# Performance work log

Hardware: AMD Instinct MI355X
Metric: run time of the kernel (lower is better)

## Reference

```python
import jax, jax.numpy as jnp
import numpy as np

B, N, D, H, A = 1024, 16, 64, 64, 64
TAU = 0.01   # gumbel-softmax temperature from the source
EPS = 1e-10


def setup_inputs() -> dict:
    key = jax.random.key(0)
    ks = jax.random.split(key, 23)

    def rn(k, shape, s=0.05):
        return jax.random.normal(k, shape, dtype=jnp.float32) * s

    return {
        "obs": jax.random.normal(ks[0], (B, N, D), dtype=jnp.float32),
        "hidden_state": jax.random.normal(ks[1], (B * N, A), dtype=jnp.float32),
        "gumbel_u": jax.random.uniform(ks[2], (B * N * (N - 1), 2), dtype=jnp.float32,
                                       minval=1e-6, maxval=1.0 - 1e-6),
        "W_enc": rn(ks[3], (D, H)), "b_enc": rn(ks[4], (H,)),
        "Wih_f": rn(ks[5], (3 * H, 2 * H)), "Whh_f": rn(ks[6], (3 * H, H)),
        "bih_f": rn(ks[7], (3 * H,)), "bhh_f": rn(ks[8], (3 * H,)),
        "Wih_b": rn(ks[9], (3 * H, 2 * H)), "Whh_b": rn(ks[10], (3 * H, H)),
        "bih_b": rn(ks[11], (3 * H,)), "bhh_b": rn(ks[12], (3 * H,)),
        "W_hard": rn(ks[13], (2 * H, 2)), "b_hard": rn(ks[14], (2,)),
        "Wq": rn(ks[15], (H, A)), "Wk": rn(ks[16], (H, A)),
        "Wv": rn(ks[17], (H, A)), "b_v": rn(ks[18], (A,)),
        "Wih_c": rn(ks[19], (3 * A, A)), "Whh_c": rn(ks[20], (3 * A, A)),
        "bih_c": rn(ks[21], (3 * A,)), "bhh_c": rn(ks[22], (3 * A,)),
    }


def _gru_scan(x_seq, Wih, Whh, bih, bhh):
    # x_seq: [T, BN, 2H]; PyTorch GRU gate order r, z, n. Input projection
    # for all timesteps is precomputed (one big GEMM) outside the scan.
    gi = jnp.einsum('tbd,gd->tbg', x_seq, Wih) + bih  # [T, BN, 3H]
    h0 = jnp.zeros((x_seq.shape[1], Whh.shape[1]), x_seq.dtype)

    def step(h, gi_t):
        gh = h @ Whh.T + bhh
        i_r, i_z, i_n = jnp.split(gi_t, 3, axis=-1)
        h_r, h_z, h_n = jnp.split(gh, 3, axis=-1)
        r = jax.nn.sigmoid(i_r + h_r)
        z = jax.nn.sigmoid(i_z + h_z)
        n = jnp.tanh(i_n + r * h_n)
        h_new = (1.0 - z) * n + z * h
        return h_new, h_new

    _, out = jax.lax.scan(step, h0, gi)
    return out  # [T, BN, H]


def _gru_cell(x, h, Wih, Whh, bih, bhh):
    gi = x @ Wih.T + bih
    gh = h @ Whh.T + bhh
    i_r, i_z, i_n = jnp.split(gi, 3, axis=-1)
    h_r, h_z, h_n = jnp.split(gh, 3, axis=-1)
    r = jax.nn.sigmoid(i_r + h_r)
    z = jax.nn.sigmoid(i_z + h_z)
    n = jnp.tanh(i_n + r * h_n)
    return (1.0 - z) * n + z * h


def reference(obs, hidden_state, gumbel_u, W_enc, b_enc,
              Wih_f, Whh_f, bih_f, bhh_f, Wih_b, Whh_b, bih_b, bhh_b,
              W_hard, b_hard, Wq, Wk, Wv, b_v,
              Wih_c, Whh_c, bih_c, bhh_c):
    b, n, d = obs.shape
    h_enc = jax.nn.relu(obs @ W_enc + b_enc)          # [B, N, H]
    h_flat = h_enc.reshape(-1, H)                      # [B*N, H]

    # static neighbor index table: row i lists all j != i
    j_idx = np.array([[j for j in range(n) if j != i] for i in range(n)])  # [N, N-1]

    # pairwise concat features, vectorized (replaces the double python loop)
    h_j = h_enc[:, j_idx]                               # [B, N, N-1, H]
    h_i = jnp.broadcast_to(h_enc[:, :, None, :], h_j.shape)
    pair = jnp.concatenate([h_i, h_j], axis=-1)        # [B, N, N-1, 2H]
    input_hard = pair.transpose(2, 0, 1, 3).reshape(n - 1, b * n, 2 * H)

    # bidirectional GRU over the N-1 neighbor axis
    out_f = _gru_scan(input_hard, Wih_f, Whh_f, bih_f, bhh_f)
    out_b = _gru_scan(input_hard[::-1], Wih_b, Whh_b, bih_b, bhh_b)[::-1]
    h_hard = jnp.concatenate([out_f, out_b], axis=-1)  # [N-1, B*N, 2H]
    h_hard = h_hard.transpose(1, 0, 2).reshape(-1, 2 * H)

    # hard gate: gumbel-softmax (soft sample, tau=0.01), take channel 1
    logits = h_hard @ W_hard + b_hard                   # [B*N*(N-1), 2]
    g = -jnp.log(-jnp.log(gumbel_u + EPS) + EPS)
    hard = jax.nn.softmax((logits + g) / TAU, axis=-1)
    hard_w = hard[:, 1].reshape(b, n, n - 1)            # [B, N, N-1]

    # scaled dot-product attention over neighbors j != i
    q = (h_flat @ Wq).reshape(b, n, A)
    k = (h_flat @ Wk).reshape(b, n, A)
    v = jax.nn.relu(h_flat @ Wv + b_v).reshape(b, n, A)
    k_j = k[:, j_idx]                                   # [B, N, N-1, A]
    v_j = v[:, j_idx]
    score = jnp.einsum('bna,bnja->bnj', q, k_j) / float(np.sqrt(A))
    soft = jax.nn.softmax(score, axis=-1)
    x = jnp.einsum('bnja,bnj->bna', v_j, soft * hard_w).reshape(b * n, A)

    return _gru_cell(x, hidden_state, Wih_c, Whh_c, bih_c, bhh_c)
```

## Files before the change

kernel.cpp:

```cpp
#include <hip/hip_runtime.h>
#include <hip/hip_bf16.h>
#include <stdint.h>

#define NNODE 16384
#define TAU_ 0.01f
#define EPSG 1e-10f

#define OFF_WENC 0
#define OFF_BENC 4096
#define OFF_WIHF_H 4160
#define OFF_WIHF_L 16448
#define OFF_WHHF_H 28736
#define OFF_BIHF 41024
#define OFF_BHHF 41216
#define OFF_WIHB_H 41408
#define OFF_WIHB_L 53696
#define OFF_WHHB_H 65984
#define OFF_BIHB 78272
#define OFF_BHHB 78464
#define OFF_WHARD 78656
#define OFF_BHARD 78912
#define OFF_WQT_H 78914
#define OFF_WQT_L 80962
#define OFF_WKT_H 83010
#define OFF_WKT_L 85058
#define OFF_WVT_H 87106
#define OFF_WVT_L 89154
#define OFF_BV 91202
#define OFF_WIHC_H 91266
#define OFF_WIHC_L 97410
#define OFF_WHHC_H 103554
#define OFF_WHHC_L 109698
#define OFF_BIHC 115842
#define OFF_BHHC 116034
#define OFF_WENCT_H 118784
#define OFF_WENCT_L 120832
#define OFF_YF 131072
#define OFF_YB (OFF_YF + 491520)
#define WS_FLOATS (OFF_YB + 491520)

typedef float  v4f __attribute__((ext_vector_type(4)));
typedef short  v8s __attribute__((ext_vector_type(8)));

__device__ __forceinline__ float rcpf(float x){ return __builtin_amdgcn_rcpf(x); }
__device__ __forceinline__ float sigf(float x){ return rcpf(1.0f + __expf(-x)); }
__device__ __forceinline__ float tanhfast(float x){ return 1.0f - 2.0f*rcpf(__expf(2.0f*x)+1.0f); }
__device__ __forceinline__ unsigned short f2bf(float f){
  __hip_bfloat16 h = __float2bfloat16(f);
  return *reinterpret_cast<unsigned short*>(&h);
}
__device__ __forceinline__ float bf2f(unsigned short u){
  union { unsigned int i; float f; } v; v.i = ((unsigned int)u) << 16; return v.f;
}

struct Prep {
  const float* s[20];
  int n[20];
  int o[20];
};
__global__ void k_prep(Prep p, float* __restrict__ ws){
  int a = blockIdx.y;
  int i = blockIdx.x * blockDim.x + threadIdx.x;
  if (i < p.n[a]) ws[p.o[a] + i] = p.s[a][i];
}

__global__ void k_prep2(const float* __restrict__ wenc,
                        const float* __restrict__ wihf, const float* __restrict__ wihb,
                        const float* __restrict__ whhf, const float* __restrict__ whhb,
                        const float* __restrict__ wq,   const float* __restrict__ wk,
                        const float* __restrict__ wv,   const float* __restrict__ wihc,
                        const float* __restrict__ whhc,
                        float* __restrict__ ws){
  int a = blockIdx.y;
  int i = blockIdx.x * blockDim.x + threadIdx.x;
  if (a == 0 || (a >= 5 && a <= 7)){
    if (i < 4096){
      const float* src = (a==0) ? wenc : (a==5) ? wq : (a==6) ? wk : wv;
      int oh = (a==0) ? OFF_WENCT_H : (a==5) ? OFF_WQT_H : (a==6) ? OFF_WKT_H : OFF_WVT_H;
      int ol = (a==0) ? OFF_WENCT_L : oh + 2048;
      float x = src[((i & 63) << 6) | (i >> 6)];
      unsigned short h = f2bf(x);
      unsigned short l = f2bf(x - bf2f(h));
      ((unsigned short*)(ws + oh))[i] = h;
      ((unsigned short*)(ws + ol))[i] = l;
    }
  } else if (a == 1 || a == 2){
    if (i < 24576){
      float x = (a == 1 ? wihf : wihb)[i];
      unsigned short h = f2bf(x);
      unsigned short l = f2bf(x - bf2f(h));
      ((unsigned short*)(ws + (a == 1 ? OFF_WIHF_H : OFF_WIHB_H)))[i] = h;
      ((unsigned short*)(ws + (a == 1 ? OFF_WIHF_L : OFF_WIHB_L)))[i] = l;
    }
  } else if (a == 3 || a == 4){
    if (i < 12288){
      float x = (a == 3 ? whhf : whhb)[i];
      ((unsigned short*)(ws + (a == 3 ? OFF_WHHF_H : OFF_WHHB_H)))[i] = f2bf(x);
    }
  } else {
    if (i < 12288){
      float x = (a == 8 ? wihc : whhc)[i];
      unsigned short h = f2bf(x);
      unsigned short l = f2bf(x - bf2f(h));
      int oh = (a == 8 ? OFF_WIHC_H : OFF_WHHC_H);
      ((unsigned short*)(ws + oh))[i] = h;
      ((unsigned short*)(ws + oh + 6144))[i] = l;
    }
  }
}

__global__ __launch_bounds__(256, 2) void k_main(const float* __restrict__ obs,
                                                 const float* __restrict__ hid,
                                                 const float* __restrict__ gum,
                                                 float* __restrict__ ws,
                                                 float* __restrict__ out){
  __shared__ float smem[10176];
  float* s_u2 = smem;
  unsigned short* s_B = (unsigned short*)(smem + 6272);
  unsigned short* s_obs_h = s_B;
  unsigned short* s_obs_l = s_B + 1152;
  float* s_red = smem + 9088;
  float* s_y   = smem + 9216;
  float* s_q  = smem;
  float* s_k  = smem + 1088;
  float* s_v  = smem + 2176;
  float* s_co = smem + 3264;

  const int tid = threadIdx.x;
  const int nl  = tid & 63;
  const int grp = __builtin_amdgcn_readfirstlane(tid >> 6);
  const int dir = grp >> 1;
  const int lw  = grp & 1;
  const int hi2 = grp;
  const int q4  = nl >> 4;
  const int i_c = nl & 15;
  const int node = i_c;
  const int base = blockIdx.x * 16;

  {
    float4 a = *(const float4*)&obs[base*64 + tid*4];
    int nn = tid >> 4, d0 = (tid & 15)*4;
    unsigned short hh[4], ll[4];
    float xs[4] = {a.x,a.y,a.z,a.w};
    #pragma unroll
    for (int e = 0; e < 4; e++){
      hh[e] = f2bf(xs[e]);
      ll[e] = f2bf(xs[e] - bf2f(hh[e]));
    }
    *(uint2*)&s_obs_h[nn*72 + d0] = make_uint2((unsigned)hh[0] | ((unsigned)hh[1]<<16),
                                               (unsigned)hh[2] | ((unsigned)hh[3]<<16));
    *(uint2*)&s_obs_l[nn*72 + d0] = make_uint2((unsigned)ll[0] | ((unsigned)ll[1]<<16),
                                               (unsigned)ll[2] | ((unsigned)ll[3]<<16));
  }
  __syncthreads();

  const float* benc = ws + OFF_BENC;
  const unsigned short* wtH = (const unsigned short*)(ws + OFF_WENCT_H);
  const unsigned short* wtL = (const unsigned short*)(ws + OFF_WENCT_L);
  v4f dEnc;
  {
    v8s obH[2], obL[2];
    #pragma unroll
    for (int kc = 0; kc < 2; kc++){
      int ba = node*72 + kc*32 + q4*8;
      obH[kc] = *(const v8s*)&s_obs_h[ba];
      obL[kc] = *(const v8s*)&s_obs_l[ba];
    }
    float4 bi = *(const float4*)&benc[16*hi2 + 4*q4];
    v4f d = (v4f){bi.x, bi.y, bi.z, bi.w};
    #pragma unroll
    for (int kc = 0; kc < 2; kc++){
      int aa = (16*hi2 + i_c)*64 + kc*32 + q4*8;
      v8s aH = *(const v8s*)&wtH[aa];
      v8s aL = *(const v8s*)&wtL[aa];
      d = __builtin_amdgcn_mfma_f32_16x16x32_bf16(aH, obH[kc], d, 0,0,0);
      d = __builtin_amdgcn_mfma_f32_16x16x32_bf16(aH, obL[kc], d, 0,0,0);
      d = __builtin_amdgcn_mfma_f32_16x16x32_bf16(aL, obH[kc], d, 0,0,0);
    }
    dEnc = d;
  }
  __syncthreads();
  {
    unsigned short hh[4], ll[4];
    #pragma unroll
    for (int r = 0; r < 4; r++){
      float v = fmaxf(dEnc[r], 0.0f);
      hh[r] = f2bf(v);
      ll[r] = f2bf(v - bf2f(hh[r]));
    }
    int wa = node*72 + 16*hi2 + 4*q4;
    *(uint2*)&s_obs_h[wa] = make_uint2((unsigned)hh[0] | ((unsigned)hh[1]<<16),
                                       (unsigned)hh[2] | ((unsigned)hh[3]<<16));
    *(uint2*)&s_obs_l[wa] = make_uint2((unsigned)ll[0] | ((unsigned)ll[1]<<16),
                                       (unsigned)ll[2] | ((unsigned)ll[3]<<16));
  }
  __syncthreads();

  v8s hbH[2], hbL[2];
  #pragma unroll
  for (int kc = 0; kc < 2; kc++){
    int ba = node*72 + kc*32 + q4*8;
    hbH[kc] = *(const v8s*)&s_obs_h[ba];
    hbL[kc] = *(const v8s*)&s_obs_l[ba];
  }

  v4f dq, dk, dv;
  {
    const unsigned short* wqH = (const unsigned short*)(ws + OFF_WQT_H);
    const unsigned short* wqL = (const unsigned short*)(ws + OFF_WQT_L);
    const unsigned short* wkH = (const unsigned short*)(ws + OFF_WKT_H);
    const unsigned short* wkL = (const unsigned short*)(ws + OFF_WKT_L);
    const unsigned short* wvH = (const unsigned short*)(ws + OFF_WVT_H);
    const unsigned short* wvL = (const unsigned short*)(ws + OFF_WVT_L);
    const float* bv = ws + OFF_BV;
    v4f q_ = (v4f){0.f,0.f,0.f,0.f};
    v4f k_ = (v4f){0.f,0.f,0.f,0.f};
    float4 b4 = *(const float4*)&bv[16*hi2 + 4*q4];
    v4f v_ = (v4f){b4.x, b4.y, b4.z, b4.w};
    #pragma unroll
    for (int kc = 0; kc < 2; kc++){
      int ai = (16*hi2 + i_c)*64 + kc*32 + q4*8;
      v8s aH = *(const v8s*)&wqH[ai]; v8s aL = *(const v8s*)&wqL[ai];
      q_ = __builtin_amdgcn_mfma_f32_16x16x32_bf16(aH, hbH[kc], q_, 0,0,0);
      q_ = __builtin_amdgcn_mfma_f32_16x16x32_bf16(aH, hbL[kc], q_, 0,0,0);
      q_ = __builtin_amdgcn_mfma_f32_16x16x32_bf16(aL, hbH[kc], q_, 0,0,0);
      aH = *(const v8s*)&wkH[ai]; aL = *(const v8s*)&wkL[ai];
      k_ = __builtin_amdgcn_mfma_f32_16x16x32_bf16(aH, hbH[kc], k_, 0,0,0);
      k_ = __builtin_amdgcn_mfma_f32_16x16x32_bf16(aH, hbL[kc], k_, 0,0,0);
      k_ = __builtin_amdgcn_mfma_f32_16x16x32_bf16(aL, hbH[kc], k_, 0,0,0);
      aH = *(const v8s*)&wvH[ai]; aL = *(const v8s*)&wvL[ai];
      v_ = __builtin_amdgcn_mfma_f32_16x16x32_bf16(aH, hbH[kc], v_, 0,0,0);
      v_ = __builtin_amdgcn_mfma_f32_16x16x32_bf16(aH, hbL[kc], v_, 0,0,0);
      v_ = __builtin_amdgcn_mfma_f32_16x16x32_bf16(aL, hbH[kc], v_, 0,0,0);
    }
    dq = q_; dk = k_; dv = v_;
  }

  const float* bih = ws + (dir ? OFF_BIHB : OFF_BIHF);
  const float* bhh = ws + (dir ? OFF_BHHB : OFF_BHHF);
  const unsigned short* wiH = (const unsigned short*)(ws + (dir ? OFF_WIHB_H : OFF_WIHF_H));
  const unsigned short* wiL = (const unsigned short*)(ws + (dir ? OFF_WIHB_L : OFF_WIHF_L));
  const unsigned short* whH = (const unsigned short*)(ws + (dir ? OFF_WHHB_H : OFF_WHHF_H));
  float* myu2 = s_u2 + dir*3136;

  #pragma unroll
  for (int m = 0; m < 6; m++){
    int T = 6*lw + m;
    v4f d = (v4f){0.f,0.f,0.f,0.f};
    #pragma unroll
    for (int kc = 0; kc < 2; kc++){
      int aa = (16*T + i_c)*128 + 64 + kc*32 + q4*8;
      v8s aH = *(const v8s*)&wiH[aa];
      v8s aL = *(const v8s*)&wiL[aa];
      d = __builtin_amdgcn_mfma_f32_16x16x32_bf16(aH, hbH[kc], d, 0,0,0);
      d = __builtin_amdgcn_mfma_f32_16x16x32_bf16(aH, hbL[kc], d, 0,0,0);
      d = __builtin_amdgcn_mfma_f32_16x16x32_bf16(aL, hbH[kc], d, 0,0,0);
    }
    *(v4f*)&myu2[node*196 + 16*T + 4*q4] = d;
  }

  v4f cbr[2], cbz[2], cbn[2], bhn4[2];
  #pragma unroll
  for (int g = 0; g < 3; g++){
    #pragma unroll
    for (int t2 = 0; t2 < 2; t2++){
      int row0 = 64*g + 32*lw + 16*t2 + 4*q4;
      float4 bi = *(const float4*)&bih[row0];
      v4f d;
      if (g < 2){
        float4 bh = *(const float4*)&bhh[row0];
        d = (v4f){bi.x+bh.x, bi.y+bh.y, bi.z+bh.z, bi.w+bh.w};
      } else {
        d = (v4f){bi.x, bi.y, bi.z, bi.w};
      }
      int T = (64*g + 32*lw + 16*t2) >> 4;
      #pragma unroll
      for (int kc = 0; kc < 2; kc++){
        int aa = (16*T + i_c)*128 + kc*32 + q4*8;
        v8s aH = *(const v8s*)&wiH[aa];
        v8s aL = *(const v8s*)&wiL[aa];
        d = __builtin_amdgcn_mfma_f32_16x16x32_bf16(aH, hbH[kc], d, 0,0,0);
        d = __builtin_amdgcn_mfma_f32_16x16x32_bf16(aH, hbL[kc], d, 0,0,0);
        d = __builtin_amdgcn_mfma_f32_16x16x32_bf16(aL, hbH[kc], d, 0,0,0);
      }
      if (g == 0) cbr[t2] = d; else if (g == 1) cbz[t2] = d; else cbn[t2] = d;
    }
  }
  #pragma unroll
  for (int t2 = 0; t2 < 2; t2++){
    int row0 = 128 + 32*lw + 16*t2 + 4*q4;
    float4 nh = *(const float4*)&bhh[row0];
    bhn4[t2] = (v4f){nh.x, nh.y, nh.z, nh.w};
  }

  v8s afr[2][2], afz[2][2], afn[2][2];
  #pragma unroll
  for (int t2 = 0; t2 < 2; t2++){
    #pragma unroll
    for (int kc = 0; kc < 2; kc++){
      #pragma unroll
      for (int g = 0; g < 3; g++){
        int row = g*64 + 32*lw + 16*t2 + i_c;
        v8s a = *(const v8s*)&whH[row*64 + kc*32 + q4*8];
        if (g == 0) afr[t2][kc] = a; else if (g == 1) afz[t2][kc] = a; else afn[t2][kc] = a;
      }
    }
  }

  const float* whard = ws + OFF_WHARD + dir*128;
  float wh0[8], wh1[8];
  #pragma unroll
  for (int t2 = 0; t2 < 2; t2++){
    #pragma unroll
    for (int r = 0; r < 4; r++){
      int l = 32*lw + 16*t2 + 4*q4 + r;
      wh0[t2*4+r] = whard[l*2];
      wh1[t2*4+r] = whard[l*2+1];
    }
  }
  __syncthreads();

  unsigned short* myh = s_B + dir*2816;
  float hv[8];
  #pragma unroll
  for (int m = 0; m < 8; m++) hv[m] = 0.0f;

  for (int kk = 0; kk < 15; kk++){
    const int t  = dir ? (14 - kk) : kk;
    const int j  = t + (t >= i_c ? 1 : 0);
    const int jl = j;
    const int rb = kk & 1;
    const int wb = (kk + 1) & 1;

    v8s b0, b1;
    if (kk > 0){
      const unsigned short* rp = myh + rb*1408 + node*88 + q4*8;
      b0 = *(const v8s*)(rp);
      b1 = *(const v8s*)(rp + 32);
    }

    float a0p = 0.f, a1p = 0.f;
    #pragma unroll
    for (int t2 = 0; t2 < 2; t2++){
      int l0 = 32*lw + 16*t2 + 4*q4;
      v4f dr = cbr[t2], dz = cbz[t2];
      v4f dn = (v4f){0.f,0.f,0.f,0.f};
      if (kk > 0){
        dr = __builtin_amdgcn_mfma_f32_16x16x32_bf16(afr[t2][0], b0, dr, 0,0,0);
        dr = __builtin_amdgcn_mfma_f32_16x16x32_bf16(afr[t2][1], b1, dr, 0,0,0);
        dz = __builtin_amdgcn_mfma_f32_16x16x32_bf16(afz[t2][0], b0, dz, 0,0,0);
        dz = __builtin_amdgcn_mfma_f32_16x16x32_bf16(afz[t2][1], b1, dz, 0,0,0);
        dn = __builtin_amdgcn_mfma_f32_16x16x32_bf16(afn[t2][0], b0, dn, 0,0,0);
        dn = __builtin_amdgcn_mfma_f32_16x16x32_bf16(afn[t2][1], b1, dn, 0,0,0);
      }
      v4f ur = *(const v4f*)&myu2[jl*196 +       l0];
      v4f uz = *(const v4f*)&myu2[jl*196 +  64 + l0];
      v4f un = *(const v4f*)&myu2[jl*196 + 128 + l0];
      float hn[4];
      #pragma unroll
      for (int r = 0; r < 4; r++){
        float rg = sigf(dr[r] + ur[r]);
        float zg = sigf(dz[r] + uz[r]);
        float ng = tanhfast(cbn[t2][r] + un[r] + rg*(bhn4[t2][r] + dn[r]));
        float hnew = (1.0f - zg)*ng + zg*hv[t2*4+r];
        hv[t2*4+r] = hnew;
        hn[r] = hnew;
        a0p += hnew*wh0[t2*4+r];
        a1p += hnew*wh1[t2*4+r];
      }
      unsigned int p0 = (unsigned int)f2bf(hn[0]) | ((unsigned int)f2bf(hn[1]) << 16);
      unsigned int p1 = (unsigned int)f2bf(hn[2]) | ((unsigned int)f2bf(hn[3]) << 16);
      *(uint2*)(myh + wb*1408 + node*88 + l0) = make_uint2(p0, p1);
    }

    a0p += __shfl_xor(a0p, 16); a0p += __shfl_xor(a0p, 32);
    a1p += __shfl_xor(a1p, 16); a1p += __shfl_xor(a1p, 32);
    float* sr = s_red + dir*64 + rb*32;
    if (lw == 0 && q4 == 0)
      *(float2*)&sr[node*2] = make_float2(a0p, a1p);
    __syncthreads();
    if (lw == 1 && q4 == 0){
      float2 pp = *(const float2*)&sr[node*2];
      *(float2*)&s_y[dir*480 + (node*15 + t)*2] = make_float2(a0p + pp.x, a1p + pp.y);
    }
  }
  __syncthreads();

  {
    *(v4f*)&s_q[node*68 + 16*hi2 + 4*q4] = dq;
    #pragma unroll
    for (int r = 0; r < 4; r++){
      s_k[(16*hi2 + 4*q4 + r)*17 + node] = dk[r];
      s_v[(16*hi2 + 4*q4 + r)*17 + node] = fmaxf(dv[r], 0.f);
    }
  }
  __syncthreads();

  const int n2  = tid >> 3;
  const int asl = tid & 7;
  if (tid < 128){
    float4 aq0 = *(const float4*)&s_q[n2*68 + asl*8];
    float4 aq1 = *(const float4*)&s_q[n2*68 + asl*8 + 4];
    float sc[15];
    #pragma unroll
    for (int t = 0; t < 15; t++){
      int jl = t + (t >= n2 ? 1 : 0);
      const float* kp = s_k + (asl*8)*17 + jl;
      float s = aq0.x*kp[0]  + aq0.y*kp[17]  + aq0.z*kp[34]  + aq0.w*kp[51]
              + aq1.x*kp[68] + aq1.y*kp[85]  + aq1.z*kp[102] + aq1.w*kp[119];
      s += __shfl_xor(s, 1); s += __shfl_xor(s, 2); s += __shfl_xor(s, 4);
      sc[t] = s * 0.125f;
    }
    float m = sc[0];
    #pragma unroll
    for (int t = 1; t < 15; t++) m = fmaxf(m, sc[t]);
    float den = 0.f;
    #pragma unroll
    for (int t = 0; t < 15; t++) den += __expf(sc[t]-m);
    float rden = rcpf(den);
    const float bh0 = ws[OFF_BHARD], bh1 = ws[OFF_BHARD+1];
    #pragma unroll
    for (int t = 0; t < 15; t++){
      if ((t & 7) == asl){
        int yi = (n2*15 + t)*2;
        float y0 = s_y[yi]     + s_y[480 + yi]     + bh0;
        float y1 = s_y[yi + 1] + s_y[480 + yi + 1] + bh1;
        float2 u2 = *(const float2*)&gum[((base + n2)*15 + t)*2];
        float g0 = -__logf(-__logf(u2.x + EPSG) + EPSG);
        float g1 = -__logf(-__logf(u2.y + EPSG) + EPSG);
        float w  = sigf(((y1+g1) - (y0+g0)) * (1.0f/TAU_));
        s_co[t*16 + n2] = __expf(sc[t]-m)*rden*w;
      }
    }
  }
  __syncthreads();

  unsigned short* s_xh  = s_B;
  unsigned short* s_xl  = s_B + 1152;
  unsigned short* s_h0h = s_B + 2304;
  unsigned short* s_h0l = s_B + 3456;
  if (tid < 128){
    float xa[8];
    #pragma unroll
    for (int il = 0; il < 8; il++) xa[il] = 0.f;
    #pragma unroll
    for (int t = 0; t < 15; t++){
      float c = s_co[t*16 + n2];
      int jl = t + (t >= n2 ? 1 : 0);
      const float* vp = s_v + (asl*8)*17 + jl;
      xa[0] += c*vp[0];   xa[1] += c*vp[17];  xa[2] += c*vp[34];  xa[3] += c*vp[51];
      xa[4] += c*vp[68];  xa[5] += c*vp[85];  xa[6] += c*vp[102]; xa[7] += c*vp[119];
    }
    union { v8s v; unsigned short u[8]; } XH, XL;
    #pragma unroll
    for (int e = 0; e < 8; e++){
      XH.u[e] = f2bf(xa[e]);
      XL.u[e] = f2bf(xa[e] - bf2f(XH.u[e]));
    }
    *(v8s*)&s_xh[n2*72 + asl*8] = XH.v;
    *(v8s*)&s_xl[n2*72 + asl*8] = XL.v;
  }
  {
    float4 a = *(const float4*)&hid[base*64 + tid*4];
    int nn = tid >> 4, d0 = (tid & 15)*4;
    unsigned short hh[4], ll[4];
    float xs[4] = {a.x,a.y,a.z,a.w};
    #pragma unroll
    for (int e = 0; e < 4; e++){
      hh[e] = f2bf(xs[e]);
      ll[e] = f2bf(xs[e] - bf2f(hh[e]));
    }
    *(uint2*)&s_h0h[nn*72 + d0] = make_uint2((unsigned)hh[0] | ((unsigned)hh[1]<<16),
                                             (unsigned)hh[2] | ((unsigned)hh[3]<<16));
    *(uint2*)&s_h0l[nn*72 + d0] = make_uint2((unsigned)ll[0] | ((unsigned)ll[1]<<16),
                                             (unsigned)ll[2] | ((unsigned)ll[3]<<16));
  }
  __syncthreads();

  {
    v8s xbH[2], xbL[2], h0H[2], h0L[2];
    #pragma unroll
    for (int kc = 0; kc < 2; kc++){
      int ba = node*72 + kc*32 + q4*8;
      xbH[kc] = *(const v8s*)&s_xh[ba];  xbL[kc] = *(const v8s*)&s_xl[ba];
      h0H[kc] = *(const v8s*)&s_h0h[ba]; h0L[kc] = *(const v8s*)&s_h0l[ba];
    }
    const unsigned short* wiH2 = (const unsigned short*)(ws + OFF_WIHC_H);
    const unsigned short* wiL2 = (const unsigned short*)(ws + OFF_WIHC_L);
    const unsigned short* whH2 = (const unsigned short*)(ws + OFF_WHHC_H);
    const unsigned short* whL2 = (const unsigned short*)(ws + OFF_WHHC_L);
    const float* bihc = ws + OFF_BIHC; const float* bhhc = ws + OFF_BHHC;
    v4f gi[3], gh[3];
    #pragma unroll
    for (int g = 0; g < 3; g++){
      int row0 = g*64 + 16*hi2 + 4*q4;
      float4 bi = *(const float4*)&bihc[row0];
      float4 bh = *(const float4*)&bhhc[row0];
      v4f di, dh;
      if (g < 2){
        di = (v4f){bi.x+bh.x, bi.y+bh.y, bi.z+bh.z, bi.w+bh.w};
        dh = (v4f){0.f,0.f,0.f,0.f};
      } else {
        di = (v4f){bi.x, bi.y, bi.z, bi.w};
        dh = (v4f){bh.x, bh.y, bh.z, bh.w};
      }
      #pragma unroll
      for (int kc = 0; kc < 2; kc++){
        int ai = (g*64 + 16*hi2 + i_c)*64 + kc*32 + q4*8;
        v8s aH = *(const v8s*)&wiH2[ai]; v8s aL = *(const v8s*)&wiL2[ai];
        di = __builtin_amdgcn_mfma_f32_16x16x32_bf16(aH, xbH[kc], di, 0,0,0);
        di = __builtin_amdgcn_mfma_f32_16x16x32_bf16(aH, xbL[kc], di, 0,0,0);
        di = __builtin_amdgcn_mfma_f32_16x16x32_bf16(aL, xbH[kc], di, 0,0,0);
        aH = *(const v8s*)&whH2[ai]; aL = *(const v8s*)&whL2[ai];
        dh = __builtin_amdgcn_mfma_f32_16x16x32_bf16(aH, h0H[kc], dh, 0,0,0);
        dh = __builtin_amdgcn_mfma_f32_16x16x32_bf16(aH, h0L[kc], dh, 0,0,0);
        dh = __builtin_amdgcn_mfma_f32_16x16x32_bf16(aL, h0H[kc], dh, 0,0,0);
      }
      gi[g] = di; gh[g] = dh;
    }
    int l0 = 16*hi2 + 4*q4;
    float4 h04 = *(const float4*)&hid[(base+node)*64 + l0];
    float hh4[4] = {h04.x, h04.y, h04.z, h04.w};
    float ho[4];
    #pragma unroll
    for (int r = 0; r < 4; r++){
      float rg = sigf(gi[0][r] + gh[0][r]);
      float zg = sigf(gi[1][r] + gh[1][r]);
      float ng = tanhfast(gi[2][r] + rg*gh[2][r]);
      ho[r] = (1.0f - zg)*ng + zg*hh4[r];
    }
    *(float4*)&out[(base+node)*64 + l0] = make_float4(ho[0], ho[1], ho[2], ho[3]);
  }
}

extern "C" void kernel_launch(void* const* d_in, const int* in_sizes, int n_in,
                              void* d_out, int out_size, void* d_ws, size_t ws_size,
                              hipStream_t stream){
  if (ws_size < (size_t)WS_FLOATS * sizeof(float)) return;
  float* ws = (float*)d_ws;
  static const int offs[20] = {OFF_WENC, OFF_BENC, 0, 0, OFF_BIHF, OFF_BHHF,
      0, 0, OFF_BIHB, OFF_BHHB, OFF_WHARD, OFF_BHARD, 0, 0, 0,
      OFF_BV, 0, 0, OFF_BIHC, OFF_BHHC};
  Prep p;
  for (int i = 0; i < 20; i++){
    p.s[i] = (const float*)d_in[3 + i];
    p.n[i] = in_sizes[3 + i];
    p.o[i] = offs[i];
  }
  p.n[2] = 0; p.n[3] = 0; p.n[6] = 0; p.n[7] = 0;
  p.n[12] = 0; p.n[13] = 0; p.n[14] = 0;
  p.n[16] = 0; p.n[17] = 0;
  hipLaunchKernelGGL(k_prep, dim3(96, 20), dim3(256), 0, stream, p, ws);
  hipLaunchKernelGGL(k_prep2, dim3(96, 10), dim3(256), 0, stream,
                     (const float*)d_in[3], (const float*)d_in[5], (const float*)d_in[9],
                     (const float*)d_in[6], (const float*)d_in[10],
                     (const float*)d_in[15], (const float*)d_in[16], (const float*)d_in[17],
                     (const float*)d_in[19], (const float*)d_in[20], ws);
  hipLaunchKernelGGL(k_main, dim3(1024), dim3(256), 0, stream,
                     (const float*)d_in[0], (const float*)d_in[1],
                     (const float*)d_in[2], ws, (float*)d_out);
}
```

Baseline: 192.4 us.

## Halve main kernel block to two waves each handling both GRU directions

Shrinks the main kernel from four waves to two per block, so each wave now processes both forward and backward GRU directions and two tiles of each projection. Interleaving the two independent recurrences inside one wave gives more instruction-level parallelism per sequential step and cuts the number of waves taking part in each barrier. The two weight-prep kernels are also merged into one launch to save launch overhead. The cost is higher register pressure per wave (launch bounds 128,1) and fewer waves available to hide latency.

```diff
diff --git a/kernel.cpp b/kernel.cpp
--- a/kernel.cpp
+++ b/kernel.cpp
@@ -58,21 +58,21 @@
   int n[20];
   int o[20];
 };
-__global__ void k_prep(Prep p, float* __restrict__ ws){
+__global__ void k_prep(Prep p,
+                       const float* __restrict__ wenc,
+                       const float* __restrict__ wihf, const float* __restrict__ wihb,
+                       const float* __restrict__ whhf, const float* __restrict__ whhb,
+                       const float* __restrict__ wq,   const float* __restrict__ wk,
+                       const float* __restrict__ wv,   const float* __restrict__ wihc,
+                       const float* __restrict__ whhc,
+                       float* __restrict__ ws){
   int a = blockIdx.y;
   int i = blockIdx.x * blockDim.x + threadIdx.x;
-  if (i < p.n[a]) ws[p.o[a] + i] = p.s[a][i];
-}
-
-__global__ void k_prep2(const float* __restrict__ wenc,
-                        const float* __restrict__ wihf, const float* __restrict__ wihb,
-                        const float* __restrict__ whhf, const float* __restrict__ whhb,
-                        const float* __restrict__ wq,   const float* __restrict__ wk,
-                        const float* __restrict__ wv,   const float* __restrict__ wihc,
-                        const float* __restrict__ whhc,
-                        float* __restrict__ ws){
-  int a = blockIdx.y;
-  int i = blockIdx.x * blockDim.x + threadIdx.x;
+  if (a < 20){
+    if (i < p.n[a]) ws[p.o[a] + i] = p.s[a][i];
+    return;
+  }
+  a -= 20;
   if (a == 0 || (a >= 5 && a <= 7)){
     if (i < 4096){
       const float* src = (a==0) ? wenc : (a==5) ? wq : (a==6) ? wk : wv;
@@ -109,7 +109,7 @@
   }
 }
 
-__global__ __launch_bounds__(256, 2) void k_main(const float* __restrict__ obs,
+__global__ __launch_bounds__(128, 1) void k_main(const float* __restrict__ obs,
                                                  const float* __restrict__ hid,
                                                  const float* __restrict__ gum,
                                                  float* __restrict__ ws,
@@ -128,36 +128,32 @@
 
   const int tid = threadIdx.x;
   const int nl  = tid & 63;
-  const int grp = __builtin_amdgcn_readfirstlane(tid >> 6);
-  const int dir = grp >> 1;
-  const int lw  = grp & 1;
-  const int hi2 = grp;
+  const int lw  = __builtin_amdgcn_readfirstlane(tid >> 6);
   const int q4  = nl >> 4;
   const int i_c = nl & 15;
   const int node = i_c;
   const int base = blockIdx.x * 16;
 
   {
-    float4 a = *(const float4*)&obs[base*64 + tid*4];
-    int nn = tid >> 4, d0 = (tid & 15)*4;
-    unsigned short hh[4], ll[4];
-    float xs[4] = {a.x,a.y,a.z,a.w};
-    #pragma unroll
-    for (int e = 0; e < 4; e++){
-      hh[e] = f2bf(xs[e]);
-      ll[e] = f2bf(xs[e] - bf2f(hh[e]));
-    }
-    *(uint2*)&s_obs_h[nn*72 + d0] = make_uint2((unsigned)hh[0] | ((unsigned)hh[1]<<16),
-                                               (unsigned)hh[2] | ((unsigned)hh[3]<<16));
-    *(uint2*)&s_obs_l[nn*72 + d0] = make_uint2((unsigned)ll[0] | ((unsigned)ll[1]<<16),
-                                               (unsigned)ll[2] | ((unsigned)ll[3]<<16));
+    float4 a = *(const float4*)&obs[base*64 + tid*8];
+    float4 b = *(const float4*)&obs[base*64 + tid*8 + 4];
+    int nn = tid >> 3, d0 = (tid & 7)*8;
+    union { v8s v; unsigned short u[8]; } H, L;
+    float xs[8] = {a.x,a.y,a.z,a.w,b.x,b.y,b.z,b.w};
+    #pragma unroll
+    for (int e = 0; e < 8; e++){
+      H.u[e] = f2bf(xs[e]);
+      L.u[e] = f2bf(xs[e] - bf2f(H.u[e]));
+    }
+    *(v8s*)&s_obs_h[nn*72 + d0] = H.v;
+    *(v8s*)&s_obs_l[nn*72 + d0] = L.v;
   }
   __syncthreads();
 
   const float* benc = ws + OFF_BENC;
   const unsigned short* wtH = (const unsigned short*)(ws + OFF_WENCT_H);
   const unsigned short* wtL = (const unsigned short*)(ws + OFF_WENCT_L);
-  v4f dEnc;
+  v4f dEnc[2];
   {
     v8s obH[2], obL[2];
     #pragma unroll
@@ -166,29 +162,35 @@
       obH[kc] = *(const v8s*)&s_obs_h[ba];
       obL[kc] = *(const v8s*)&s_obs_l[ba];
     }
-    float4 bi = *(const float4*)&benc[16*hi2 + 4*q4];
-    v4f d = (v4f){bi.x, bi.y, bi.z, bi.w};
-    #pragma unroll
-    for (int kc = 0; kc < 2; kc++){
-      int aa = (16*hi2 + i_c)*64 + kc*32 + q4*8;
-      v8s aH = *(const v8s*)&wtH[aa];
-      v8s aL = *(const v8s*)&wtL[aa];
-      d = __builtin_amdgcn_mfma_f32_16x16x32_bf16(aH, obH[kc], d, 0,0,0);
-      d = __builtin_amdgcn_mfma_f32_16x16x32_bf16(aH, obL[kc], d, 0,0,0);
-      d = __builtin_amdgcn_mfma_f32_16x16x32_bf16(aL, obH[kc], d, 0,0,0);
-    }
-    dEnc = d;
-  }
-  __syncthreads();
-  {
+    #pragma unroll
+    for (int tt = 0; tt < 2; tt++){
+      int lT = 2*lw + tt;
+      float4 bi = *(const float4*)&benc[16*lT + 4*q4];
+      v4f d = (v4f){bi.x, bi.y, bi.z, bi.w};
+      #pragma unroll
+      for (int kc = 0; kc < 2; kc++){
+        int aa = (16*lT + i_c)*64 + kc*32 + q4*8;
+        v8s aH = *(const v8s*)&wtH[aa];
+        v8s aL = *(const v8s*)&wtL[aa];
+        d = __builtin_amdgcn_mfma_f32_16x16x32_bf16(aH, obH[kc], d, 0,0,0);
+        d = __builtin_amdgcn_mfma_f32_16x16x32_bf16(aH, obL[kc], d, 0,0,0);
+        d = __builtin_amdgcn_mfma_f32_16x16x32_bf16(aL, obH[kc], d, 0,0,0);
+      }
+      dEnc[tt] = d;
+    }
+  }
+  __syncthreads();
+  #pragma unroll
+  for (int tt = 0; tt < 2; tt++){
+    int lT = 2*lw + tt;
     unsigned short hh[4], ll[4];
     #pragma unroll
     for (int r = 0; r < 4; r++){
-      float v = fmaxf(dEnc[r], 0.0f);
+      float v = fmaxf(dEnc[tt][r], 0.0f);
       hh[r] = f2bf(v);
       ll[r] = f2bf(v - bf2f(hh[r]));
     }
-    int wa = node*72 + 16*hi2 + 4*q4;
+    int wa = node*72 + 16*lT + 4*q4;
     *(uint2*)&s_obs_h[wa] = make_uint2((unsigned)hh[0] | ((unsigned)hh[1]<<16),
                                        (unsigned)hh[2] | ((unsigned)hh[3]<<16));
     *(uint2*)&s_obs_l[wa] = make_uint2((unsigned)ll[0] | ((unsigned)ll[1]<<16),
@@ -204,7 +206,7 @@
     hbL[kc] = *(const v8s*)&s_obs_l[ba];
   }
 
-  v4f dq, dk, dv;
+  v4f dq[2], dk[2], dv[2];
   {
     const unsigned short* wqH = (const unsigned short*)(ws + OFF_WQT_H);
     const unsigned short* wqL = (const unsigned short*)(ws + OFF_WQT_L);
@@ -213,192 +215,218 @@
     const unsigned short* wvH = (const unsigned short*)(ws + OFF_WVT_H);
     const unsigned short* wvL = (const unsigned short*)(ws + OFF_WVT_L);
     const float* bv = ws + OFF_BV;
-    v4f q_ = (v4f){0.f,0.f,0.f,0.f};
-    v4f k_ = (v4f){0.f,0.f,0.f,0.f};
-    float4 b4 = *(const float4*)&bv[16*hi2 + 4*q4];
-    v4f v_ = (v4f){b4.x, b4.y, b4.z, b4.w};
-    #pragma unroll
-    for (int kc = 0; kc < 2; kc++){
-      int ai = (16*hi2 + i_c)*64 + kc*32 + q4*8;
-      v8s aH = *(const v8s*)&wqH[ai]; v8s aL = *(const v8s*)&wqL[ai];
-      q_ = __builtin_amdgcn_mfma_f32_16x16x32_bf16(aH, hbH[kc], q_, 0,0,0);
-      q_ = __builtin_amdgcn_mfma_f32_16x16x32_bf16(aH, hbL[kc], q_, 0,0,0);
-      q_ = __builtin_amdgcn_mfma_f32_16x16x32_bf16(aL, hbH[kc], q_, 0,0,0);
-      aH = *(const v8s*)&wkH[ai]; aL = *(const v8s*)&wkL[ai];
-      k_ = __builtin_amdgcn_mfma_f32_16x16x32_bf16(aH, hbH[kc], k_, 0,0,0);
-      k_ = __builtin_amdgcn_mfma_f32_16x16x32_bf16(aH, hbL[kc], k_, 0,0,0);
-      k_ = __builtin_amdgcn_mfma_f32_16x16x32_bf16(aL, hbH[kc], k_, 0,0,0);
-      aH = *(const v8s*)&wvH[ai]; aL = *(const v8s*)&wvL[ai];
-      v_ = __builtin_amdgcn_mfma_f32_16x16x32_bf16(aH, hbH[kc], v_, 0,0,0);
-      v_ = __builtin_amdgcn_mfma_f32_16x16x32_bf16(aH, hbL[kc], v_, 0,0,0);
-      v_ = __builtin_amdgcn_mfma_f32_16x16x32_bf16(aL, hbH[kc], v_, 0,0,0);
-    }
-    dq = q_; dk = k_; dv = v_;
-  }
-
-  const float* bih = ws + (dir ? OFF_BIHB : OFF_BIHF);
-  const float* bhh = ws + (dir ? OFF_BHHB : OFF_BHHF);
-  const unsigned short* wiH = (const unsigned short*)(ws + (dir ? OFF_WIHB_H : OFF_WIHF_H));
-  const unsigned short* wiL = (const unsigned short*)(ws + (dir ? OFF_WIHB_L : OFF_WIHF_L));
-  const unsigned short* whH = (const unsigned short*)(ws + (dir ? OFF_WHHB_H : OFF_WHHF_H));
-  float* myu2 = s_u2 + dir*3136;
-
+    #pragma unroll
+    for (int a2 = 0; a2 < 2; a2++){
+      int aT = 2*lw + a2;
+      v4f q_ = (v4f){0.f,0.f,0.f,0.f};
+      v4f k_ = (v4f){0.f,0.f,0.f,0.f};
+      float4 b4 = *(const float4*)&bv[16*aT + 4*q4];
+      v4f v_ = (v4f){b4.x, b4.y, b4.z, b4.w};
+      #pragma unroll
+      for (int kc = 0; kc < 2; kc++){
+        int ai = (16*aT + i_c)*64 + kc*32 + q4*8;
+        v8s aH = *(const v8s*)&wqH[ai]; v8s aL = *(const v8s*)&wqL[ai];
+        q_ = __builtin_amdgcn_mfma_f32_16x16x32_bf16(aH, hbH[kc], q_, 0,0,0);
+        q_ = __builtin_amdgcn_mfma_f32_16x16x32_bf16(aH, hbL[kc], q_, 0,0,0);
+        q_ = __builtin_amdgcn_mfma_f32_16x16x32_bf16(aL, hbH[kc], q_, 0,0,0);
+        aH = *(const v8s*)&wkH[ai]; aL = *(const v8s*)&wkL[ai];
+        k_ = __builtin_amdgcn_mfma_f32_16x16x32_bf16(aH, hbH[kc], k_, 0,0,0);
+        k_ = __builtin_amdgcn_mfma_f32_16x16x32_bf16(aH, hbL[kc], k_, 0,0,0);
+        k_ = __builtin_amdgcn_mfma_f32_16x16x32_bf16(aL, hbH[kc], k_, 0,0,0);
+        aH = *(const v8s*)&wvH[ai]; aL = *(const v8s*)&wvL[ai];
+        v_ = __builtin_amdgcn_mfma_f32_16x16x32_bf16(aH, hbH[kc], v_, 0,0,0);
+        v_ = __builtin_amdgcn_mfma_f32_16x16x32_bf16(aH, hbL[kc], v_, 0,0,0);
+        v_ = __builtin_amdgcn_mfma_f32_16x16x32_bf16(aL, hbH[kc], v_, 0,0,0);
+      }
+      dq[a2] = q_; dk[a2] = k_; dv[a2] = v_;
+    }
+  }
+
+  v4f cbr[2][2], cbz[2][2], cbn[2][2], bhn4[2][2];
+  v8s afr[2][2][2], afz[2][2][2], afn[2][2][2];
+  float wh0[2][8], wh1[2][8];
   #pragma unroll
-  for (int m = 0; m < 6; m++){
-    int T = 6*lw + m;
-    v4f d = (v4f){0.f,0.f,0.f,0.f};
-    #pragma unroll
-    for (int kc = 0; kc < 2; kc++){
-      int aa = (16*T + i_c)*128 + 64 + kc*32 + q4*8;
-      v8s aH = *(const v8s*)&wiH[aa];
-      v8s aL = *(const v8s*)&wiL[aa];
-      d = __builtin_amdgcn_mfma_f32_16x16x32_bf16(aH, hbH[kc], d, 0,0,0);
-      d = __builtin_amdgcn_mfma_f32_16x16x32_bf16(aH, hbL[kc], d, 0,0,0);
-      d = __builtin_amdgcn_mfma_f32_16x16x32_bf16(aL, hbH[kc], d, 0,0,0);
-    }
-    *(v4f*)&myu2[node*196 + 16*T + 4*q4] = d;
-  }
-
-  v4f cbr[2], cbz[2], cbn[2], bhn4[2];
-  #pragma unroll
-  for (int g = 0; g < 3; g++){
-    #pragma unroll
-    for (int t2 = 0; t2 < 2; t2++){
-      int row0 = 64*g + 32*lw + 16*t2 + 4*q4;
-      float4 bi = *(const float4*)&bih[row0];
-      v4f d;
-      if (g < 2){
-        float4 bh = *(const float4*)&bhh[row0];
-        d = (v4f){bi.x+bh.x, bi.y+bh.y, bi.z+bh.z, bi.w+bh.w};
-      } else {
-        d = (v4f){bi.x, bi.y, bi.z, bi.w};
-      }
-      int T = (64*g + 32*lw + 16*t2) >> 4;
+  for (int dd = 0; dd < 2; dd++){
+    const float* bih = ws + (dd ? OFF_BIHB : OFF_BIHF);
+    const float* bhh = ws + (dd ? OFF_BHHB : OFF_BHHF);
+    const unsigned short* wiH = (const unsigned short*)(ws + (dd ? OFF_WIHB_H : OFF_WIHF_H));
+    const unsigned short* wiL = (const unsigned short*)(ws + (dd ? OFF_WIHB_L : OFF_WIHF_L));
+    const unsigned short* whHd = (const unsigned short*)(ws + (dd ? OFF_WHHB_H : OFF_WHHF_H));
+    float* u2d = s_u2 + dd*3136;
+
+    #pragma unroll
+    for (int m = 0; m < 6; m++){
+      int T = 6*lw + m;
+      v4f d = (v4f){0.f,0.f,0.f,0.f};
       #pragma unroll
       for (int kc = 0; kc < 2; kc++){
-        int aa = (16*T + i_c)*128 + kc*32 + q4*8;
+        int aa = (16*T + i_c)*128 + 64 + kc*32 + q4*8;
         v8s aH = *(const v8s*)&wiH[aa];
         v8s aL = *(const v8s*)&wiL[aa];
         d = __builtin_amdgcn_mfma_f32_16x16x32_bf16(aH, hbH[kc], d, 0,0,0);
         d = __builtin_amdgcn_mfma_f32_16x16x32_bf16(aH, hbL[kc], d, 0,0,0);
         d = __builtin_amdgcn_mfma_f32_16x16x32_bf16(aL, hbH[kc], d, 0,0,0);
       }
-      if (g == 0) cbr[t2] = d; else if (g == 1) cbz[t2] = d; else cbn[t2] = d;
-    }
-  }
+      *(v4f*)&u2d[node*196 + 16*T + 4*q4] = d;
+    }
+
+    #pragma unroll
+    for (int g = 0; g < 3; g++){
+      #pragma unroll
+      for (int t2 = 0; t2 < 2; t2++){
+        int row0 = 64*g + 32*lw + 16*t2 + 4*q4;
+        float4 bi = *(const float4*)&bih[row0];
+        v4f d;
+        if (g < 2){
+          float4 bh = *(const float4*)&bhh[row0];
+          d = (v4f){bi.x+bh.x, bi.y+bh.y, bi.z+bh.z, bi.w+bh.w};
+        } else {
+          d = (v4f){bi.x, bi.y, bi.z, bi.w};
+        }
+        int T = (64*g + 32*lw + 16*t2) >> 4;
+        #pragma unroll
+        for (int kc = 0; kc < 2; kc++){
+          int aa = (16*T + i_c)*128 + kc*32 + q4*8;
+          v8s aH = *(const v8s*)&wiH[aa];
+          v8s aL = *(const v8s*)&wiL[aa];
+          d = __builtin_amdgcn_mfma_f32_16x16x32_bf16(aH, hbH[kc], d, 0,0,0);
+          d = __builtin_amdgcn_mfma_f32_16x16x32_bf16(aH, hbL[kc], d, 0,0,0);
+          d = __builtin_amdgcn_mfma_f32_16x16x32_bf16(aL, hbH[kc], d, 0,0,0);
+        }
+        if (g == 0) cbr[dd][t2] = d; else if (g == 1) cbz[dd][t2] = d; else cbn[dd][t2] = d;
+      }
+    }
+    #pragma unroll
+    for (int t2 = 0; t2 < 2; t2++){
+      int row0 = 128 + 32*lw + 16*t2 + 4*q4;
+      float4 nh = *(const float4*)&bhh[row0];
+      bhn4[dd][t2] = (v4f){nh.x, nh.y, nh.z, nh.w};
+    }
+
+    #pragma unroll
+    for (int t2 = 0; t2 < 2; t2++){
+      #pragma unroll
+      for (int kc = 0; kc < 2; kc++){
+        #pragma unroll
+        for (int g = 0; g < 3; g++){
+          int row = g*64 + 32*lw + 16*t2 + i_c;
+          v8s a = *(const v8s*)&whHd[row*64 + kc*32 + q4*8];
+          if (g == 0) afr[dd][t2][kc] = a;
+          else if (g == 1) afz[dd][t2][kc] = a;
+          else afn[dd][t2][kc] = a;
+        }
+      }
+    }
+
+    const float* whard = ws + OFF_WHARD + dd*128;
+    #pragma unroll
+    for (int t2 = 0; t2 < 2; t2++){
+      #pragma unroll
+      for (int r = 0; r < 4; r++){
+        int l = 32*lw + 16*t2 + 4*q4 + r;
+        wh0[dd][t2*4+r] = whard[l*2];
+        wh1[dd][t2*4+r] = whard[l*2+1];
+      }
+    }
+  }
+  __syncthreads();
+
+  float hv[2][8];
   #pragma unroll
-  for (int t2 = 0; t2 < 2; t2++){
-    int row0 = 128 + 32*lw + 16*t2 + 4*q4;
-    float4 nh = *(const float4*)&bhh[row0];
-    bhn4[t2] = (v4f){nh.x, nh.y, nh.z, nh.w};
-  }
-
-  v8s afr[2][2], afz[2][2], afn[2][2];
-  #pragma unroll
-  for (int t2 = 0; t2 < 2; t2++){
-    #pragma unroll
-    for (int kc = 0; kc < 2; kc++){
-      #pragma unroll
-      for (int g = 0; g < 3; g++){
-        int row = g*64 + 32*lw + 16*t2 + i_c;
-        v8s a = *(const v8s*)&whH[row*64 + kc*32 + q4*8];
-        if (g == 0) afr[t2][kc] = a; else if (g == 1) afz[t2][kc] = a; else afn[t2][kc] = a;
-      }
-    }
-  }
-
-  const float* whard = ws + OFF_WHARD + dir*128;
-  float wh0[8], wh1[8];
-  #pragma unroll
-  for (int t2 = 0; t2 < 2; t2++){
-    #pragma unroll
-    for (int r = 0; r < 4; r++){
-      int l = 32*lw + 16*t2 + 4*q4 + r;
-      wh0[t2*4+r] = whard[l*2];
-      wh1[t2*4+r] = whard[l*2+1];
-    }
-  }
-  __syncthreads();
-
-  unsigned short* myh = s_B + dir*2816;
-  float hv[8];
-  #pragma unroll
-  for (int m = 0; m < 8; m++) hv[m] = 0.0f;
+  for (int dd = 0; dd < 2; dd++)
+    #pragma unroll
+    for (int m = 0; m < 8; m++) hv[dd][m] = 0.0f;
 
   for (int kk = 0; kk < 15; kk++){
-    const int t  = dir ? (14 - kk) : kk;
-    const int j  = t + (t >= i_c ? 1 : 0);
-    const int jl = j;
     const int rb = kk & 1;
     const int wb = (kk + 1) & 1;
-
-    v8s b0, b1;
+    const int tt0 = kk;
+    const int tt1 = 14 - kk;
+
+    v8s b0[2], b1[2];
     if (kk > 0){
-      const unsigned short* rp = myh + rb*1408 + node*88 + q4*8;
-      b0 = *(const v8s*)(rp);
-      b1 = *(const v8s*)(rp + 32);
-    }
-
-    float a0p = 0.f, a1p = 0.f;
-    #pragma unroll
-    for (int t2 = 0; t2 < 2; t2++){
-      int l0 = 32*lw + 16*t2 + 4*q4;
-      v4f dr = cbr[t2], dz = cbz[t2];
-      v4f dn = (v4f){0.f,0.f,0.f,0.f};
-      if (kk > 0){
-        dr = __builtin_amdgcn_mfma_f32_16x16x32_bf16(afr[t2][0], b0, dr, 0,0,0);
-        dr = __builtin_amdgcn_mfma_f32_16x16x32_bf16(afr[t2][1], b1, dr, 0,0,0);
-        dz = __builtin_amdgcn_mfma_f32_16x16x32_bf16(afz[t2][0], b0, dz, 0,0,0);
-        dz = __builtin_amdgcn_mfma_f32_16x16x32_bf16(afz[t2][1], b1, dz, 0,0,0);
-        dn = __builtin_amdgcn_mfma_f32_16x16x32_bf16(afn[t2][0], b0, dn, 0,0,0);
-        dn = __builtin_amdgcn_mfma_f32_16x16x32_bf16(afn[t2][1], b1, dn, 0,0,0);
-      }
-      v4f ur = *(const v4f*)&myu2[jl*196 +       l0];
-      v4f uz = *(const v4f*)&myu2[jl*196 +  64 + l0];
-      v4f un = *(const v4f*)&myu2[jl*196 + 128 + l0];
-      float hn[4];
-      #pragma unroll
-      for (int r = 0; r < 4; r++){
-        float rg = sigf(dr[r] + ur[r]);
-        float zg = sigf(dz[r] + uz[r]);
-        float ng = tanhfast(cbn[t2][r] + un[r] + rg*(bhn4[t2][r] + dn[r]));
-        float hnew = (1.0f - zg)*ng + zg*hv[t2*4+r];
-        hv[t2*4+r] = hnew;
-        hn[r] = hnew;
-        a0p += hnew*wh0[t2*4+r];
-        a1p += hnew*wh1[t2*4+r];
-      }
-      unsigned int p0 = (unsigned int)f2bf(hn[0]) | ((unsigned int)f2bf(hn[1]) << 16);
-      unsigned int p1 = (unsigned int)f2bf(hn[2]) | ((unsigned int)f2bf(hn[3]) << 16);
-      *(uint2*)(myh + wb*1408 + node*88 + l0) = make_uint2(p0, p1);
-    }
-
-    a0p += __shfl_xor(a0p, 16); a0p += __shfl_xor(a0p, 32);
-    a1p += __shfl_xor(a1p, 16); a1p += __shfl_xor(a1p, 32);
-    float* sr = s_red + dir*64 + rb*32;
-    if (lw == 0 && q4 == 0)
-      *(float2*)&sr[node*2] = make_float2(a0p, a1p);
+      #pragma unroll
+      for (int dd = 0; dd < 2; dd++){
+        const unsigned short* rp = s_B + dd*2816 + rb*1408 + node*88 + q4*8;
+        b0[dd] = *(const v8s*)(rp);
+        b1[dd] = *(const v8s*)(rp + 32);
+      }
+    }
+
+    float a0p[2] = {0.f, 0.f}, a1p[2] = {0.f, 0.f};
+    #pragma unroll
+    for (int dd = 0; dd < 2; dd++){
+      const int t  = dd ? tt1 : tt0;
+      const int jl = t + (t >= i_c ? 1 : 0);
+      const float* u2d = s_u2 + dd*3136;
+      #pragma unroll
+      for (int t2 = 0; t2 < 2; t2++){
+        int l0 = 32*lw + 16*t2 + 4*q4;
+        v4f dr = cbr[dd][t2], dz = cbz[dd][t2];
+        v4f dn = (v4f){0.f,0.f,0.f,0.f};
+        if (kk > 0){
+          dr = __builtin_amdgcn_mfma_f32_16x16x32_bf16(afr[dd][t2][0], b0[dd], dr, 0,0,0);
+          dr = __builtin_amdgcn_mfma_f32_16x16x32_bf16(afr[dd][t2][1], b1[dd], dr, 0,0,0);
+          dz = __builtin_amdgcn_mfma_f32_16x16x32_bf16(afz[dd][t2][0], b0[dd], dz, 0,0,0);
+          dz = __builtin_amdgcn_mfma_f32_16x16x32_bf16(afz[dd][t2][1], b1[dd], dz, 0,0,0);
+          dn = __builtin_amdgcn_mfma_f32_16x16x32_bf16(afn[dd][t2][0], b0[dd], dn, 0,0,0);
+          dn = __builtin_amdgcn_mfma_f32_16x16x32_bf16(afn[dd][t2][1], b1[dd], dn, 0,0,0);
+        }
+        v4f ur = *(const v4f*)&u2d[jl*196 +       l0];
+        v4f uz = *(const v4f*)&u2d[jl*196 +  64 + l0];
+        v4f un = *(const v4f*)&u2d[jl*196 + 128 + l0];
+        float hn[4];
+        #pragma unroll
+        for (int r = 0; r < 4; r++){
+          float rg = sigf(dr[r] + ur[r]);
+          float zg = sigf(dz[r] + uz[r]);
+          float ng = tanhfast(cbn[dd][t2][r] + un[r] + rg*(bhn4[dd][t2][r] + dn[r]));
+          float hnew = (1.0f - zg)*ng + zg*hv[dd][t2*4+r];
+          hv[dd][t2*4+r] = hnew;
+          hn[r] = hnew;
+          a0p[dd] += hnew*wh0[dd][t2*4+r];
+          a1p[dd] += hnew*wh1[dd][t2*4+r];
+        }
+        unsigned int p0 = (unsigned int)f2bf(hn[0]) | ((unsigned int)f2bf(hn[1]) << 16);
+        unsigned int p1 = (unsigned int)f2bf(hn[2]) | ((unsigned int)f2bf(hn[3]) << 16);
+        *(uint2*)(s_B + dd*2816 + wb*1408 + node*88 + l0) = make_uint2(p0, p1);
+      }
+    }
+
+    #pragma unroll
+    for (int dd = 0; dd < 2; dd++){
+      a0p[dd] += __shfl_xor(a0p[dd], 16); a0p[dd] += __shfl_xor(a0p[dd], 32);
+      a1p[dd] += __shfl_xor(a1p[dd], 16); a1p[dd] += __shfl_xor(a1p[dd], 32);
+    }
+    if (lw == 0 && q4 == 0){
+      *(float2*)&s_red[       rb*32 + node*2] = make_float2(a0p[0], a1p[0]);
+      *(float2*)&s_red[64   + rb*32 + node*2] = make_float2(a0p[1], a1p[1]);
+    }
     __syncthreads();
     if (lw == 1 && q4 == 0){
-      float2 pp = *(const float2*)&sr[node*2];
-      *(float2*)&s_y[dir*480 + (node*15 + t)*2] = make_float2(a0p + pp.x, a1p + pp.y);
-    }
-  }
-  __syncthreads();
-
-  {
-    *(v4f*)&s_q[node*68 + 16*hi2 + 4*q4] = dq;
+      float2 p0 = *(const float2*)&s_red[       rb*32 + node*2];
+      float2 p1 = *(const float2*)&s_red[64   + rb*32 + node*2];
+      *(float2*)&s_y[      (node*15 + tt0)*2] = make_float2(a0p[0] + p0.x, a1p[0] + p0.y);
+      *(float2*)&s_y[480 + (node*15 + tt1)*2] = make_float2(a0p[1] + p1.x, a1p[1] + p1.y);
+    }
+  }
+  __syncthreads();
+
+  #pragma unroll
+  for (int a2 = 0; a2 < 2; a2++){
+    int aT = 2*lw + a2;
+    *(v4f*)&s_q[node*68 + 16*aT + 4*q4] = dq[a2];
     #pragma unroll
     for (int r = 0; r < 4; r++){
-      s_k[(16*hi2 + 4*q4 + r)*17 + node] = dk[r];
-      s_v[(16*hi2 + 4*q4 + r)*17 + node] = fmaxf(dv[r], 0.f);
+      s_k[(16*aT + 4*q4 + r)*17 + node] = dk[a2][r];
+      s_v[(16*aT + 4*q4 + r)*17 + node] = fmaxf(dv[a2][r], 0.f);
     }
   }
   __syncthreads();
 
   const int n2  = tid >> 3;
   const int asl = tid & 7;
-  if (tid < 128){
+  {
     float4 aq0 = *(const float4*)&s_q[n2*68 + asl*8];
     float4 aq1 = *(const float4*)&s_q[n2*68 + asl*8 + 4];
     float sc[15];
@@ -439,7 +467,7 @@
   unsigned short* s_xl  = s_B + 1152;
   unsigned short* s_h0h = s_B + 2304;
   unsigned short* s_h0l = s_B + 3456;
-  if (tid < 128){
+  {
     float xa[8];
     #pragma unroll
     for (int il = 0; il < 8; il++) xa[il] = 0.f;
@@ -461,19 +489,18 @@
     *(v8s*)&s_xl[n2*72 + asl*8] = XL.v;
   }
   {
-    float4 a = *(const float4*)&hid[base*64 + tid*4];
-    int nn = tid >> 4, d0 = (tid & 15)*4;
-    unsigned short hh[4], ll[4];
-    float xs[4] = {a.x,a.y,a.z,a.w};
-    #pragma unroll
-    for (int e = 0; e < 4; e++){
-      hh[e] = f2bf(xs[e]);
-      ll[e] = f2bf(xs[e] - bf2f(hh[e]));
-    }
-    *(uint2*)&s_h0h[nn*72 + d0] = make_uint2((unsigned)hh[0] | ((unsigned)hh[1]<<16),
-                                             (unsigned)hh[2] | ((unsigned)hh[3]<<16));
-    *(uint2*)&s_h0l[nn*72 + d0] = make_uint2((unsigned)ll[0] | ((unsigned)ll[1]<<16),
-                                             (unsigned)ll[2] | ((unsigned)ll[3]<<16));
+    float4 a = *(const float4*)&hid[base*64 + tid*8];
+    float4 b = *(const float4*)&hid[base*64 + tid*8 + 4];
+    int nn = tid >> 3, d0 = (tid & 7)*8;
+    union { v8s v; unsigned short u[8]; } H, L;
+    float xs[8] = {a.x,a.y,a.z,a.w,b.x,b.y,b.z,b.w};
+    #pragma unroll
+    for (int e = 0; e < 8; e++){
+      H.u[e] = f2bf(xs[e]);
+      L.u[e] = f2bf(xs[e] - bf2f(H.u[e]));
+    }
+    *(v8s*)&s_h0h[nn*72 + d0] = H.v;
+    *(v8s*)&s_h0l[nn*72 + d0] = L.v;
   }
   __syncthreads();
 
@@ -490,46 +517,53 @@
     const unsigned short* whH2 = (const unsigned short*)(ws + OFF_WHHC_H);
     const unsigned short* whL2 = (const unsigned short*)(ws + OFF_WHHC_L);
     const float* bihc = ws + OFF_BIHC; const float* bhhc = ws + OFF_BHHC;
-    v4f gi[3], gh[3];
+    v4f gi[3][2], gh[3][2];
     #pragma unroll
     for (int g = 0; g < 3; g++){
-      int row0 = g*64 + 16*hi2 + 4*q4;
-      float4 bi = *(const float4*)&bihc[row0];
-      float4 bh = *(const float4*)&bhhc[row0];
-      v4f di, dh;
-      if (g < 2){
-        di = (v4f){bi.x+bh.x, bi.y+bh.y, bi.z+bh.z, bi.w+bh.w};
-        dh = (v4f){0.f,0.f,0.f,0.f};
-      } else {
-        di = (v4f){bi.x, bi.y, bi.z, bi.w};
-        dh = (v4f){bh.x, bh.y, bh.z, bh.w};
-      }
-      #pragma unroll
-      for (int kc = 0; kc < 2; kc++){
-        int ai = (g*64 + 16*hi2 + i_c)*64 + kc*32 + q4*8;
-        v8s aH = *(const v8s*)&wiH2[ai]; v8s aL = *(const v8s*)&wiL2[ai];
-        di = __builtin_amdgcn_mfma_f32_16x16x32_bf16(aH, xbH[kc], di, 0,0,0);
-        di = __builtin_amdgcn_mfma_f32_16x16x32_bf16(aH, xbL[kc], di, 0,0,0);
-        di = __builtin_amdgcn_mfma_f32_16x16x32_bf16(aL, xbH[kc], di, 0,0,0);
-        aH = *(const v8s*)&whH2[ai]; aL = *(const v8s*)&whL2[ai];
-        dh = __builtin_amdgcn_mfma_f32_16x16x32_bf16(aH, h0H[kc], dh, 0,0,0);
-        dh = __builtin_amdgcn_mfma_f32_16x16x32_bf16(aH, h0L[kc], dh, 0,0,0);
-        dh = __builtin_amdgcn_mfma_f32_16x16x32_bf16(aL, h0H[kc], dh, 0,0,0);
-      }
-      gi[g] = di; gh[g] = dh;
-    }
-    int l0 = 16*hi2 + 4*q4;
-    float4 h04 = *(const float4*)&hid[(base+node)*64 + l0];
-    float hh4[4] = {h04.x, h04.y, h04.z, h04.w};
-    float ho[4];
-    #pragma unroll
-    for (int r = 0; r < 4; r++){
-      float rg = sigf(gi[0][r] + gh[0][r]);
-      float zg = sigf(gi[1][r] + gh[1][r]);
-      float ng = tanhfast(gi[2][r] + rg*gh[2][r]);
-      ho[r] = (1.0f - zg)*ng + zg*hh4[r];
-    }
-    *(float4*)&out[(base+node)*64 + l0] = make_float4(ho[0], ho[1], ho[2], ho[3]);
+      #pragma unroll
+      for (int uu = 0; uu < 2; uu++){
+        int u = 2*lw + uu;
+        int row0 = g*64 + 16*u + 4*q4;
+        float4 bi = *(const float4*)&bihc[row0];
+        float4 bh = *(const float4*)&bhhc[row0];
+        v4f di, dh;
+        if (g < 2){
+          di = (v4f){bi.x+bh.x, bi.y+bh.y, bi.z+bh.z, bi.w+bh.w};
+          dh = (v4f){0.f,0.f,0.f,0.f};
+        } else {
+          di = (v4f){bi.x, bi.y, bi.z, bi.w};
+          dh = (v4f){bh.x, bh.y, bh.z, bh.w};
+        }
+        #pragma unroll
+        for (int kc = 0; kc < 2; kc++){
+          int ai = (g*64 + 16*u + i_c)*64 + kc*32 + q4*8;
+          v8s aH = *(const v8s*)&wiH2[ai]; v8s aL = *(const v8s*)&wiL2[ai];
+          di = __builtin_amdgcn_mfma_f32_16x16x32_bf16(aH, xbH[kc], di, 0,0,0);
+          di = __builtin_amdgcn_mfma_f32_16x16x32_bf16(aH, xbL[kc], di, 0,0,0);
+          di = __builtin_amdgcn_mfma_f32_16x16x32_bf16(aL, xbH[kc], di, 0,0,0);
+          aH = *(const v8s*)&whH2[ai]; aL = *(const v8s*)&whL2[ai];
+          dh = __builtin_amdgcn_mfma_f32_16x16x32_bf16(aH, h0H[kc], dh, 0,0,0);
+          dh = __builtin_amdgcn_mfma_f32_16x16x32_bf16(aH, h0L[kc], dh, 0,0,0);
+          dh = __builtin_amdgcn_mfma_f32_16x16x32_bf16(aL, h0H[kc], dh, 0,0,0);
+        }
+        gi[g][uu] = di; gh[g][uu] = dh;
+      }
+    }
+    #pragma unroll
+    for (int uu = 0; uu < 2; uu++){
+      int l0 = 16*(2*lw + uu) + 4*q4;
+      float4 h04 = *(const float4*)&hid[(base+node)*64 + l0];
+      float hh4[4] = {h04.x, h04.y, h04.z, h04.w};
+      float ho[4];
+      #pragma unroll
+      for (int r = 0; r < 4; r++){
+        float rg = sigf(gi[0][uu][r] + gh[0][uu][r]);
+        float zg = sigf(gi[1][uu][r] + gh[1][uu][r]);
+        float ng = tanhfast(gi[2][uu][r] + rg*gh[2][uu][r]);
+        ho[r] = (1.0f - zg)*ng + zg*hh4[r];
+      }
+      *(float4*)&out[(base+node)*64 + l0] = make_float4(ho[0], ho[1], ho[2], ho[3]);
+    }
   }
 }
 
@@ -550,13 +584,12 @@
   p.n[2] = 0; p.n[3] = 0; p.n[6] = 0; p.n[7] = 0;
   p.n[12] = 0; p.n[13] = 0; p.n[14] = 0;
   p.n[16] = 0; p.n[17] = 0;
-  hipLaunchKernelGGL(k_prep, dim3(96, 20), dim3(256), 0, stream, p, ws);
-  hipLaunchKernelGGL(k_prep2, dim3(96, 10), dim3(256), 0, stream,
+  hipLaunchKernelGGL(k_prep, dim3(96, 30), dim3(256), 0, stream, p,
                      (const float*)d_in[3], (const float*)d_in[5], (const float*)d_in[9],
                      (const float*)d_in[6], (const float*)d_in[10],
                      (const float*)d_in[15], (const float*)d_in[16], (const float*)d_in[17],
                      (const float*)d_in[19], (const float*)d_in[20], ws);
-  hipLaunchKernelGGL(k_main, dim3(1024), dim3(256), 0, stream,
+  hipLaunchKernelGGL(k_main, dim3(1024), dim3(128), 0, stream,
                      (const float*)d_in[0], (const float*)d_in[1],
                      (const float*)d_in[2], ws, (float*)d_out);
 }
```

Result: slower. 208.0 us (+8.1%).
